# Optimization experiments

Hardware: AMD Instinct MI355X
Metric: run time of the kernel (lower is better)

Reference implementation:

```python
import jax, jax.numpy as jnp
import numpy as np

B, H, S, D = 2, 16, 2048, 128
ALIBI_MAX_BIAS = 8.0


def alibi_bias(seq_len: int, num_heads: int):
    # slopes = 2 ** -(start, 2*start, ..., num_heads*start), start = max_bias / num_heads
    start = ALIBI_MAX_BIAS / num_heads
    slopes = jnp.exp2(-(jnp.arange(1, num_heads + 1, dtype=jnp.float32) * start))  # [H]
    dist = (jnp.arange(seq_len)[None, :] - jnp.arange(seq_len)[:, None]).astype(jnp.float32)  # [S,S] j-i
    return (dist[None, :, :] * slopes[:, None, None])[None]  # [1,H,S,S]


def setup_inputs() -> dict:
    key = jax.random.key(0)
    kq, kk, kv = jax.random.split(key, 3)
    q = jax.random.normal(kq, (B, H, S, D), dtype=jnp.float32)
    k = jax.random.normal(kk, (B, H, S, D), dtype=jnp.float32)
    v = jax.random.normal(kv, (B, H, S, D), dtype=jnp.float32)
    mask = jnp.tril(jnp.ones((S, S), dtype=jnp.int32))[None, None]  # causal [1,1,S,S]
    return {"q": q, "k": k, "v": v, "mask": mask}


def reference(q, k, v, mask):
    dim = q.shape[-1]
    scale = jnp.sqrt(jnp.asarray(dim, dtype=q.dtype))
    alibi = alibi_bias(k.shape[-2], k.shape[-3]).astype(q.dtype)
    mat = jnp.einsum("bhsd,bhtd->bhst", q, k) / scale + alibi  # [B,H,S,S]
    mat = jnp.where(mask == 0, jnp.asarray(-1000000.0, dtype=mat.dtype), mat)
    mat = jax.nn.softmax(mat, axis=-1)
    return jnp.einsum("bhst,bhtd->bhsd", mat, v)
```

## Files before the change

### kernel.cpp

```cpp
#include <hip/hip_runtime.h>
#include <hip/hip_bf16.h>

typedef short s16x8 __attribute__((ext_vector_type(8)));
typedef float f32x16 __attribute__((ext_vector_type(16)));

#define LOG2E 1.44269504088896f

__device__ __forceinline__ unsigned bfpack2(float lo, float hi) {
  unsigned a = (unsigned)__builtin_bit_cast(unsigned short, __float2bfloat16(lo));
  unsigned b = (unsigned)__builtin_bit_cast(unsigned short, __float2bfloat16(hi));
  return a | (b << 16);
}

union U4 { unsigned u[4]; uint4 q; s16x8 v; };

__global__ __launch_bounds__(128)
void prep_kv(const float* __restrict__ Kg, const float* __restrict__ Vg,
             char* __restrict__ tiles) {
  constexpr int S = 2048, Dh = 128;
  const int g  = (int)blockIdx.x;
  const int bh = g >> 6, t = g & 63;
  const size_t base = (size_t)bh * S * Dh + (size_t)(t << 5) * Dh;
  char* out = tiles + ((size_t)g << 14);
  const int tid = (int)threadIdx.x;
  const int lane = tid & 63, half = tid >> 6;
  const int l31 = lane & 31, h5 = lane >> 5;

  {
    const float* krow = Kg + base + (size_t)l31 * Dh;
    #pragma unroll
    for (int i = 0; i < 4; ++i) {
      const int ks = half * 4 + i;
      const float* p = krow + 16 * ks + 8 * h5;
      float4 a = *(const float4*)p;
      float4 b = *(const float4*)(p + 4);
      U4 w;
      w.u[0] = bfpack2(a.x, a.y); w.u[1] = bfpack2(a.z, a.w);
      w.u[2] = bfpack2(b.x, b.y); w.u[3] = bfpack2(b.z, b.w);
      *(uint4*)(out + ks * 1024 + lane * 16) = w.q;
    }
  }
  __shared__ float lds[32][132];
  {
    const int rv = tid >> 2, q4 = tid & 3;
    const float* vrow = Vg + base + (size_t)rv * Dh;
    #pragma unroll
    for (int p = 0; p < 8; ++p)
      *(float4*)(&lds[rv][q4 * 4 + p * 16]) = *(const float4*)(vrow + q4 * 4 + p * 16);
  }
  __syncthreads();
  {
    #pragma unroll
    for (int i = 0; i < 4; ++i) {
      const int gp = half * 4 + i;
      const int ks = gp >> 2, dt = gp & 3;
      const int cv = 2 * ks + h5, d = 32 * dt + l31;
      U4 w;
      #pragma unroll
      for (int u = 0; u < 4; ++u)
        w.u[u] = bfpack2(lds[8 * cv + 2 * u][d], lds[8 * cv + 2 * u + 1][d]);
      *(uint4*)(out + 8192 + gp * 1024 + lane * 16) = w.q;
    }
  }
}

__global__ __launch_bounds__(128, 2)
void attn_alibi(const float* __restrict__ Qg, float* __restrict__ Og,
                const char* __restrict__ tiles) {
  constexpr int S = 2048, Dh = 128;
  const int lid  = (int)blockIdx.x;
  const int xcd  = lid & 7;
  const int u    = lid >> 3;
  const int bh   = xcd + 8 * (u >> 5);
  const int pr   = u & 31;
  const int head = bh & 15;

  const int tid  = (int)threadIdx.x;
  const int wq   = tid >> 6;
  const int lane = tid & 63, l31 = lane & 31, h5 = lane >> 5;

  const float c1     = 0.08838834764831845f * LOG2E;
  const float slope2 = exp2f(-0.5f * (float)(head + 1)) * LOG2E;

  const char* tb = tiles + (((size_t)bh << 6) << 14);

  float cpat[16];
  #pragma unroll
  for (int r = 0; r < 16; ++r)
    cpat[r] = slope2 * (float)((r & 3) + 8 * (r >> 2) + 4 * h5);

  __shared__ float olds[4][64][17];
  __shared__ float mlds[2][2][32];

  for (int ph = 0; ph < 2; ++ph) {
    const int qt = ph ? (63 - pr) : pr;
    const int iq = (qt << 5) + l31;

    s16x8 qf[8];
    {
      const float* qrow = Qg + (size_t)bh * S * Dh + (size_t)iq * Dh;
      #pragma unroll
      for (int ks = 0; ks < 8; ++ks) {
        const float* p = qrow + 16 * ks + 8 * h5;
        float4 a = *(const float4*)p;
        float4 b = *(const float4*)(p + 4);
        U4 w;
        w.u[0] = bfpack2(a.x, a.y); w.u[1] = bfpack2(a.z, a.w);
        w.u[2] = bfpack2(b.x, b.y); w.u[3] = bfpack2(b.z, b.w);
        qf[ks] = w.v;
      }
    }

    f32x16 oacc[4];
    #pragma unroll
    for (int dt = 0; dt < 4; ++dt)
      #pragma unroll
      for (int r = 0; r < 16; ++r) oacc[dt][r] = 0.0f;
    float m2 = -3.0e38f, lsum = 0.0f;

    const int nt = qt + 1;
    for (int t = wq; t < nt; t += 2) {
      const char* kb = tb + ((size_t)t << 14) + lane * 16;
      s16x8 kf[8], vf[8];
      #pragma unroll
      for (int ks = 0; ks < 8; ++ks)
        kf[ks] = *(const s16x8*)(kb + ks * 1024);
      #pragma unroll
      for (int gp = 0; gp < 8; ++gp)
        vf[gp] = *(const s16x8*)(kb + 8192 + gp * 1024);

      f32x16 sc;
      #pragma unroll
      for (int r = 0; r < 16; ++r) sc[r] = 0.0f;
      __builtin_amdgcn_s_setprio(1);
      #pragma unroll
      for (int ks = 0; ks < 8; ++ks)
        sc = __builtin_amdgcn_mfma_f32_32x32x16_bf16(kf[ks], qf[ks], sc, 0, 0, 0);
      __builtin_amdgcn_s_setprio(0);

      const float sb = slope2 * (float)((t << 5) - iq);
      float mloc = -3.0e38f;
      if (t != qt) {
        #pragma unroll
        for (int r = 0; r < 16; ++r) {
          float v = fmaf(sc[r], c1, sb + cpat[r]);
          sc[r] = v;
          mloc = fmaxf(mloc, v);
        }
      } else {
        #pragma unroll
        for (int r = 0; r < 16; ++r) {
          const float b = sb + cpat[r];
          float v = fmaf(sc[r], c1, b);
          v = (b > 0.0f) ? -3.0e38f : v;
          sc[r] = v;
          mloc = fmaxf(mloc, v);
        }
      }
      mloc = fmaxf(mloc, __shfl_xor(mloc, 32));
      if (!__all(mloc <= m2 + 8.0f)) {
        const float mnew = fmaxf(m2, mloc);
        const float corr = __builtin_amdgcn_exp2f(m2 - mnew);
        m2 = mnew;
        lsum *= corr;
        #pragma unroll
        for (int dt = 0; dt < 4; ++dt)
          #pragma unroll
          for (int r = 0; r < 16; ++r) oacc[dt][r] *= corr;
      }
      float ps = 0.0f;
      #pragma unroll
      for (int r = 0; r < 16; ++r) {
        const float p = __builtin_amdgcn_exp2f(sc[r] - m2);
        sc[r] = p;
        ps += p;
      }
      lsum += ps;

      unsigned pk[4][2];
      #pragma unroll
      for (int rg = 0; rg < 4; ++rg) {
        pk[rg][0] = bfpack2(sc[4 * rg + 0], sc[4 * rg + 1]);
        pk[rg][1] = bfpack2(sc[4 * rg + 2], sc[4 * rg + 3]);
      }

      #pragma unroll
      for (int ks = 0; ks < 2; ++ks) {
        unsigned a0 = pk[2 * ks][0], b0 = pk[2 * ks + 1][0];
        unsigned a1 = pk[2 * ks][1], b1 = pk[2 * ks + 1][1];
        asm("v_permlane32_swap_b32 %0, %1" : "+v"(a0), "+v"(b0));
        asm("v_permlane32_swap_b32 %0, %1" : "+v"(a1), "+v"(b1));
        U4 bf;
        bf.u[0] = a0; bf.u[1] = a1; bf.u[2] = b0; bf.u[3] = b1;
        __builtin_amdgcn_s_setprio(1);
        #pragma unroll
        for (int dt = 0; dt < 4; ++dt)
          oacc[dt] = __builtin_amdgcn_mfma_f32_32x32x16_bf16(
              vf[4 * ks + dt], bf.v, oacc[dt], 0, 0, 0);
        __builtin_amdgcn_s_setprio(0);
      }
    }

    lsum += __shfl_xor(lsum, 32);
    #pragma unroll
    for (int dtL = 0; dtL < 2; ++dtL) {
      const int dt = 2 * (1 - wq) + dtL;
      #pragma unroll
      for (int r = 0; r < 16; ++r) olds[dt][lane][r] = oacc[dt][r];
    }
    mlds[wq][0][l31] = m2;
    mlds[wq][1][l31] = lsum;
    __syncthreads();
    {
      const float pm = mlds[1 - wq][0][l31];
      const float pl = mlds[1 - wq][1][l31];
      const float ms = fmaxf(m2, pm);
      const float so = __builtin_amdgcn_exp2f(m2 - ms);
      const float sp = __builtin_amdgcn_exp2f(pm - ms);
      const float rl = 1.0f / (lsum * so + pl * sp);
      float* orow = Og + (size_t)bh * S * Dh + (size_t)iq * Dh;
      #pragma unroll
      for (int dtL = 0; dtL < 2; ++dtL) {
        const int dt = 2 * wq + dtL;
        #pragma unroll
        for (int rg = 0; rg < 4; ++rg) {
          float4 v;
          v.x = (oacc[dt][4 * rg + 0] * so + olds[dt][lane][4 * rg + 0] * sp) * rl;
          v.y = (oacc[dt][4 * rg + 1] * so + olds[dt][lane][4 * rg + 1] * sp) * rl;
          v.z = (oacc[dt][4 * rg + 2] * so + olds[dt][lane][4 * rg + 2] * sp) * rl;
          v.w = (oacc[dt][4 * rg + 3] * so + olds[dt][lane][4 * rg + 3] * sp) * rl;
          *(float4*)(orow + 32 * dt + 8 * rg + 4 * h5) = v;
        }
      }
    }
    __syncthreads();
  }
}

extern "C" void kernel_launch(void* const* d_in, const int* in_sizes, int n_in,
                              void* d_out, int out_size, void* d_ws, size_t ws_size,
                              hipStream_t stream) {
  (void)in_sizes; (void)n_in; (void)out_size; (void)ws_size;
  const float* q = (const float*)d_in[0];
  const float* k = (const float*)d_in[1];
  const float* v = (const float*)d_in[2];
  float* o = (float*)d_out;
  char* tiles = (char*)d_ws;
  prep_kv<<<dim3(2048), dim3(128), 0, stream>>>(k, v, tiles);
  attn_alibi<<<dim3(1024), dim3(128), 0, stream>>>(q, o, tiles);
}
```

Measured before the change: 95.09 us.

## Double-buffer K tile loads and stage output through LDS for coalesced stores

The KV loop is unrolled by two with ping-pong K register buffers, so the next tile's K fragments load while the current tile's QK^T and softmax run. V is still loaded per step. The output epilogue now writes the normalized results into a shared-memory tile first, then the whole block stores full rows with coalesced float4 writes. This costs extra registers (a second K buffer), which may reduce occupancy under the 128x2 launch bounds, plus about 17KB more LDS and an extra barrier.

Result: slower. 102.9 us (+8.2%).

```diff
diff --git a/kernel.cpp b/kernel.cpp
--- a/kernel.cpp
+++ b/kernel.cpp
@@ -91,6 +91,90 @@
 
   __shared__ float olds[4][64][17];
   __shared__ float mlds[2][2][32];
+  __shared__ __align__(16) float fin[32][132];
+
+#define LOADK(KF, T) do {                                                     \
+    const char* kb_ = tb + ((size_t)(T) << 14) + lane * 16;                   \
+    _Pragma("unroll")                                                         \
+    for (int ks_ = 0; ks_ < 8; ++ks_)                                         \
+      KF[ks_] = *(const s16x8*)(kb_ + ks_ * 1024);                            \
+  } while (0)
+
+#define STEP(KF, KFN, T) do {                                                 \
+    const char* vb_ = tb + ((size_t)(T) << 14) + 8192 + lane * 16;            \
+    s16x8 vf[8];                                                              \
+    _Pragma("unroll")                                                         \
+    for (int gp_ = 0; gp_ < 8; ++gp_)                                         \
+      vf[gp_] = *(const s16x8*)(vb_ + gp_ * 1024);                            \
+    if ((T) + 2 < nt) LOADK(KFN, (T) + 2);                                    \
+    f32x16 sc;                                                                \
+    _Pragma("unroll")                                                         \
+    for (int r = 0; r < 16; ++r) sc[r] = 0.0f;                                \
+    __builtin_amdgcn_s_setprio(1);                                            \
+    _Pragma("unroll")                                                         \
+    for (int ks = 0; ks < 8; ++ks)                                            \
+      sc = __builtin_amdgcn_mfma_f32_32x32x16_bf16(KF[ks], qf[ks], sc, 0, 0, 0); \
+    __builtin_amdgcn_s_setprio(0);                                            \
+    const float sb = slope2 * (float)(((T) << 5) - iq);                       \
+    float mloc = -3.0e38f;                                                    \
+    if ((T) != qt) {                                                          \
+      _Pragma("unroll")                                                       \
+      for (int r = 0; r < 16; ++r) {                                          \
+        float v = fmaf(sc[r], c1, sb + cpat[r]);                              \
+        sc[r] = v;                                                            \
+        mloc = fmaxf(mloc, v);                                                \
+      }                                                                       \
+    } else {                                                                  \
+      _Pragma("unroll")                                                       \
+      for (int r = 0; r < 16; ++r) {                                          \
+        const float b = sb + cpat[r];                                         \
+        float v = fmaf(sc[r], c1, b);                                         \
+        v = (b > 0.0f) ? -3.0e38f : v;                                        \
+        sc[r] = v;                                                            \
+        mloc = fmaxf(mloc, v);                                                \
+      }                                                                       \
+    }                                                                         \
+    mloc = fmaxf(mloc, __shfl_xor(mloc, 32));                                 \
+    if (!__all(mloc <= m2 + 8.0f)) {                                          \
+      const float mnew = fmaxf(m2, mloc);                                     \
+      const float corr = __builtin_amdgcn_exp2f(m2 - mnew);                   \
+      m2 = mnew;                                                              \
+      lsum *= corr;                                                           \
+      _Pragma("unroll")                                                       \
+      for (int dt = 0; dt < 4; ++dt)                                          \
+        _Pragma("unroll")                                                     \
+        for (int r = 0; r < 16; ++r) oacc[dt][r] *= corr;                     \
+    }                                                                         \
+    float ps = 0.0f;                                                          \
+    _Pragma("unroll")                                                         \
+    for (int r = 0; r < 16; ++r) {                                            \
+      const float p = __builtin_amdgcn_exp2f(sc[r] - m2);                     \
+      sc[r] = p;                                                              \
+      ps += p;                                                                \
+    }                                                                         \
+    lsum += ps;                                                               \
+    unsigned pk[4][2];                                                        \
+    _Pragma("unroll")                                                         \
+    for (int rg = 0; rg < 4; ++rg) {                                          \
+      pk[rg][0] = bfpack2(sc[4 * rg + 0], sc[4 * rg + 1]);                    \
+      pk[rg][1] = bfpack2(sc[4 * rg + 2], sc[4 * rg + 3]);                    \
+    }                                                                         \
+    _Pragma("unroll")                                                         \
+    for (int ks = 0; ks < 2; ++ks) {                                          \
+      unsigned a0 = pk[2 * ks][0], b0 = pk[2 * ks + 1][0];                    \
+      unsigned a1 = pk[2 * ks][1], b1 = pk[2 * ks + 1][1];                    \
+      asm("v_permlane32_swap_b32 %0, %1" : "+v"(a0), "+v"(b0));               \
+      asm("v_permlane32_swap_b32 %0, %1" : "+v"(a1), "+v"(b1));               \
+      U4 bf;                                                                  \
+      bf.u[0] = a0; bf.u[1] = a1; bf.u[2] = b0; bf.u[3] = b1;                 \
+      __builtin_amdgcn_s_setprio(1);                                          \
+      _Pragma("unroll")                                                       \
+      for (int dt = 0; dt < 4; ++dt)                                          \
+        oacc[dt] = __builtin_amdgcn_mfma_f32_32x32x16_bf16(                   \
+            vf[4 * ks + dt], bf.v, oacc[dt], 0, 0, 0);                        \
+      __builtin_amdgcn_s_setprio(0);                                          \
+    }                                                                         \
+  } while (0)
 
   for (int ph = 0; ph < 2; ++ph) {
     const int qt = ph ? (63 - pr) : pr;
@@ -119,86 +203,11 @@
     float m2 = -3.0e38f, lsum = 0.0f;
 
     const int nt = qt + 1;
-    for (int t = wq; t < nt; t += 2) {
-      const char* kb = tb + ((size_t)t << 14) + lane * 16;
-      s16x8 kf[8], vf[8];
-      #pragma unroll
-      for (int ks = 0; ks < 8; ++ks)
-        kf[ks] = *(const s16x8*)(kb + ks * 1024);
-      #pragma unroll
-      for (int gp = 0; gp < 8; ++gp)
-        vf[gp] = *(const s16x8*)(kb + 8192 + gp * 1024);
-
-      f32x16 sc;
-      #pragma unroll
-      for (int r = 0; r < 16; ++r) sc[r] = 0.0f;
-      __builtin_amdgcn_s_setprio(1);
-      #pragma unroll
-      for (int ks = 0; ks < 8; ++ks)
-        sc = __builtin_amdgcn_mfma_f32_32x32x16_bf16(kf[ks], qf[ks], sc, 0, 0, 0);
-      __builtin_amdgcn_s_setprio(0);
-
-      const float sb = slope2 * (float)((t << 5) - iq);
-      float mloc = -3.0e38f;
-      if (t != qt) {
-        #pragma unroll
-        for (int r = 0; r < 16; ++r) {
-          float v = fmaf(sc[r], c1, sb + cpat[r]);
-          sc[r] = v;
-          mloc = fmaxf(mloc, v);
-        }
-      } else {
-        #pragma unroll
-        for (int r = 0; r < 16; ++r) {
-          const float b = sb + cpat[r];
-          float v = fmaf(sc[r], c1, b);
-          v = (b > 0.0f) ? -3.0e38f : v;
-          sc[r] = v;
-          mloc = fmaxf(mloc, v);
-        }
-      }
-      mloc = fmaxf(mloc, __shfl_xor(mloc, 32));
-      if (!__all(mloc <= m2 + 8.0f)) {
-        const float mnew = fmaxf(m2, mloc);
-        const float corr = __builtin_amdgcn_exp2f(m2 - mnew);
-        m2 = mnew;
-        lsum *= corr;
-        #pragma unroll
-        for (int dt = 0; dt < 4; ++dt)
-          #pragma unroll
-          for (int r = 0; r < 16; ++r) oacc[dt][r] *= corr;
-      }
-      float ps = 0.0f;
-      #pragma unroll
-      for (int r = 0; r < 16; ++r) {
-        const float p = __builtin_amdgcn_exp2f(sc[r] - m2);
-        sc[r] = p;
-        ps += p;
-      }
-      lsum += ps;
-
-      unsigned pk[4][2];
-      #pragma unroll
-      for (int rg = 0; rg < 4; ++rg) {
-        pk[rg][0] = bfpack2(sc[4 * rg + 0], sc[4 * rg + 1]);
-        pk[rg][1] = bfpack2(sc[4 * rg + 2], sc[4 * rg + 3]);
-      }
-
-      #pragma unroll
-      for (int ks = 0; ks < 2; ++ks) {
-        unsigned a0 = pk[2 * ks][0], b0 = pk[2 * ks + 1][0];
-        unsigned a1 = pk[2 * ks][1], b1 = pk[2 * ks + 1][1];
-        asm("v_permlane32_swap_b32 %0, %1" : "+v"(a0), "+v"(b0));
-        asm("v_permlane32_swap_b32 %0, %1" : "+v"(a1), "+v"(b1));
-        U4 bf;
-        bf.u[0] = a0; bf.u[1] = a1; bf.u[2] = b0; bf.u[3] = b1;
-        __builtin_amdgcn_s_setprio(1);
-        #pragma unroll
-        for (int dt = 0; dt < 4; ++dt)
-          oacc[dt] = __builtin_amdgcn_mfma_f32_32x32x16_bf16(
-              vf[4 * ks + dt], bf.v, oacc[dt], 0, 0, 0);
-        __builtin_amdgcn_s_setprio(0);
-      }
+    s16x8 kA[8], kB[8];
+    if (wq < nt) LOADK(kA, wq);
+    for (int t = wq; t < nt; t += 4) {
+      STEP(kA, kB, t);
+      if (t + 2 < nt) STEP(kB, kA, t + 2);
     }
 
     lsum += __shfl_xor(lsum, 32);
@@ -218,7 +227,6 @@
       const float so = __builtin_amdgcn_exp2f(m2 - ms);
       const float sp = __builtin_amdgcn_exp2f(pm - ms);
       const float rl = 1.0f / (lsum * so + pl * sp);
-      float* orow = Og + (size_t)bh * S * Dh + (size_t)iq * Dh;
       #pragma unroll
       for (int dtL = 0; dtL < 2; ++dtL) {
         const int dt = 2 * wq + dtL;
@@ -229,12 +237,25 @@
           v.y = (oacc[dt][4 * rg + 1] * so + olds[dt][lane][4 * rg + 1] * sp) * rl;
           v.z = (oacc[dt][4 * rg + 2] * so + olds[dt][lane][4 * rg + 2] * sp) * rl;
           v.w = (oacc[dt][4 * rg + 3] * so + olds[dt][lane][4 * rg + 3] * sp) * rl;
-          *(float4*)(orow + 32 * dt + 8 * rg + 4 * h5) = v;
+          *(float4*)(&fin[l31][32 * dt + 8 * rg + 4 * h5]) = v;
         }
       }
     }
     __syncthreads();
-  }
+    {
+      float* obase = Og + (size_t)bh * S * Dh + ((size_t)qt << 5) * Dh;
+      #pragma unroll
+      for (int i = 0; i < 8; ++i) {
+        const int chunk = tid + 128 * i;
+        const int row = chunk >> 5, col = chunk & 31;
+        float4 v = *(const float4*)(&fin[row][col * 4]);
+        *(float4*)(obase + row * Dh + col * 4) = v;
+      }
+    }
+    __syncthreads();
+  }
+#undef STEP
+#undef LOADK
 }
 
 extern "C" void kernel_launch(void* const* d_in, const int* in_sizes, int n_in,
```
